# Kernel optimization log

Hardware: AMD Instinct MI355X
Metric: run time of the kernel (lower is better)

## Reference

```python
import jax, jax.numpy as jnp
import numpy as np

D_IN = 1024
D_OUT = 1024

def setup_inputs() -> dict:
    key = jax.random.key(0)
    kx, kq, kk, kv = jax.random.split(key, 4)
    x = jax.random.normal(kx, (4, 4096, D_IN), dtype=jnp.float32)
    s = 1.0 / np.sqrt(D_IN)
    Wq = jax.random.uniform(kq, (D_IN, D_OUT), dtype=jnp.float32, minval=-s, maxval=s)
    Wk = jax.random.uniform(kk, (D_IN, D_OUT), dtype=jnp.float32, minval=-s, maxval=s)
    Wv = jax.random.uniform(kv, (D_IN, D_OUT), dtype=jnp.float32, minval=-s, maxval=s)
    return {"x": x, "Wq": Wq, "Wk": Wk, "Wv": Wv}

def reference(x, Wq, Wk, Wv):
    # x: [B, S, d_in]; single-head causal attention (dropout p=0 => identity)
    B, S, _ = x.shape
    Q = jnp.einsum('bsd,de->bse', x, Wq)
    K = jnp.einsum('bsd,de->bse', x, Wk)
    V = jnp.einsum('bsd,de->bse', x, Wv)
    scale = 1.0 / jnp.sqrt(jnp.asarray(K.shape[-1], dtype=Q.dtype))
    scores = jnp.einsum('bqe,bke->bqk', Q, K) * scale  # [B, S, S]
    causal = jnp.tril(jnp.ones((S, S), dtype=bool))     # mask upper triangle (diag=1)
    scores = jnp.where(causal, scores, -jnp.inf)
    weights = jax.nn.softmax(scores, axis=-1)
    return jnp.einsum('bqk,bke->bqe', weights, V)
```

## Files before the change

### kernel.cpp

```cpp
#include <hip/hip_runtime.h>
#include <hip/hip_bf16.h>
#include <stdint.h>

typedef short short8 __attribute__((ext_vector_type(8)));
typedef short short4v __attribute__((ext_vector_type(4)));
typedef float f32x4 __attribute__((ext_vector_type(4)));

static __device__ __forceinline__ short f2bf(float f) {
  union { float f; uint32_t u; } v; v.f = f;
  uint32_t r = (v.u + 0x7fffu + ((v.u >> 16) & 1u)) >> 16;
  return (short)(uint16_t)r;
}
static __device__ __forceinline__ float bf2f(short h) {
  union { uint32_t u; float f; } v; v.u = ((uint32_t)(uint16_t)h) << 16;
  return v.f;
}

#define MFMA(a, b, c) __builtin_amdgcn_mfma_f32_16x16x32_bf16((a), (b), (c), 0, 0, 0)

static __device__ __forceinline__ void gload16(const short* g, short* l) {
  __builtin_amdgcn_global_load_lds(
      (const __attribute__((address_space(1))) void*)g,
      (__attribute__((address_space(3))) void*)l, 16, 0, 0);
}

static __device__ __forceinline__ void gemm256_ring(
    const short* __restrict__ Ag, int lda,
    const short* __restrict__ Bg, int ldb, int kext,
    short* lds, int t, f32x4 (&acc)[8][4])
{
  const int w = t >> 6, lane = t & 63;
  const int lr = lane & 15, lk = lane >> 4;
  const int wm = w >> 2, wn = w & 3;
  const int nk = kext >> 5;

  const int i0 = t, i1 = 512 + t;
  const int r0 = i0 >> 2, c0 = (i0 & 3) ^ ((r0 >> 1) & 3);
  const int r1 = i1 >> 2, c1 = (i1 & 3) ^ ((r1 >> 1) & 3);
  const short* a0 = Ag + (size_t)r0 * lda + c0 * 8;
  const short* a1 = Ag + (size_t)r1 * lda + c1 * 8;
  const short* b0 = Bg + (size_t)r0 * ldb + c0 * 8;
  const short* b1 = Bg + (size_t)r1 * ldb + c1 * 8;
  const int chq = (lk ^ ((lr >> 1) & 3)) * 8;

#pragma unroll
  for (int p = 0; p < 3; ++p) {
    short* slot = lds + p * 16384;
    gload16(a0 + p * 32, slot + w * 512);
    gload16(a1 + p * 32, slot + 4096 + w * 512);
    gload16(b0 + p * 32, slot + 8192 + w * 512);
    gload16(b1 + p * 32, slot + 12288 + w * 512);
  }
  asm volatile("s_waitcnt vmcnt(8)" ::: "memory");
  __builtin_amdgcn_s_barrier();

  for (int tt = 0; tt < nk; ++tt) {
    short* slot  = lds + (tt & 3) * 16384;
    short* nslot = lds + ((tt + 3) & 3) * 16384;
    const int kk = (tt + 3) << 5;
    const bool st = (tt + 3) < nk;
    short8 bfr[4];

    short8 af[4];
#pragma unroll
    for (int mt = 0; mt < 4; ++mt) {
      int rl = wm * 128 + mt * 16 + lr;
      af[mt] = *(const short8*)&slot[rl * 32 + chq];
    }
#pragma unroll
    for (int nt = 0; nt < 4; ++nt) {
      int rl = wn * 64 + nt * 16 + lr;
      bfr[nt] = *(const short8*)&slot[8192 + rl * 32 + chq];
    }
    if (st) {
      gload16(a0 + kk, nslot + w * 512);
      gload16(a1 + kk, nslot + 4096 + w * 512);
    }
    __builtin_amdgcn_s_barrier();
    asm volatile("s_waitcnt lgkmcnt(0)" ::: "memory");
    __builtin_amdgcn_sched_barrier(0);
    __builtin_amdgcn_s_setprio(1);
#pragma unroll
    for (int mt = 0; mt < 4; ++mt)
#pragma unroll
      for (int nt = 0; nt < 4; ++nt)
        acc[mt][nt] = MFMA(af[mt], bfr[nt], acc[mt][nt]);
    __builtin_amdgcn_s_setprio(0);
    __builtin_amdgcn_s_barrier();

#pragma unroll
    for (int mt = 0; mt < 4; ++mt) {
      int rl = wm * 128 + (4 + mt) * 16 + lr;
      af[mt] = *(const short8*)&slot[rl * 32 + chq];
    }
    if (st) {
      gload16(b0 + kk, nslot + 8192 + w * 512);
      gload16(b1 + kk, nslot + 12288 + w * 512);
    }
    __builtin_amdgcn_s_barrier();
    asm volatile("s_waitcnt lgkmcnt(0)" ::: "memory");
    __builtin_amdgcn_sched_barrier(0);
    __builtin_amdgcn_s_setprio(1);
#pragma unroll
    for (int mt = 0; mt < 4; ++mt)
#pragma unroll
      for (int nt = 0; nt < 4; ++nt)
        acc[4 + mt][nt] = MFMA(af[mt], bfr[nt], acc[4 + mt][nt]);
    __builtin_amdgcn_s_setprio(0);
    const int rem = nk - 1 - tt;
    if (rem >= 3)      { asm volatile("s_waitcnt vmcnt(8)" ::: "memory"); }
    else if (rem == 2) { asm volatile("s_waitcnt vmcnt(4)" ::: "memory"); }
    else if (rem == 1) { asm volatile("s_waitcnt vmcnt(0)" ::: "memory"); }
    __builtin_amdgcn_s_barrier();
  }
}

static __device__ __forceinline__ void gemm_tile128(
    const short* __restrict__ Ag, int lda,
    const short* __restrict__ Bg, int ldb, int kext,
    short* Alds, short* Blds, int w, int lane, f32x4 (&acc)[4][4])
{
  const int wr = (w >> 1) * 64, wc = (w & 1) * 64;
  const int lr = lane & 15, lk = lane >> 4;

  const int c0 = w * 128 + lane;
  const int c1 = c0 + 64;
  const int r0 = c0 >> 2, cg0 = (c0 & 3) ^ ((r0 >> 1) & 3);
  const int r1 = c1 >> 2, cg1 = (c1 & 3) ^ ((r1 >> 1) & 3);
  const short* a0 = Ag + (size_t)r0 * lda + cg0 * 8;
  const short* a1 = Ag + (size_t)r1 * lda + cg1 * 8;
  const short* b0 = Bg + (size_t)r0 * ldb + cg0 * 8;
  const short* b1 = Bg + (size_t)r1 * ldb + cg1 * 8;
  short* la0 = Alds + w * 1024;
  short* la1 = la0 + 512;
  short* lb0 = Blds + w * 1024;
  short* lb1 = lb0 + 512;

  int ra[4], rb[4];
#pragma unroll
  for (int mt = 0; mt < 4; ++mt) {
    int rl = wr + mt * 16 + lr;
    ra[mt] = rl * 32 + (lk ^ ((rl >> 1) & 3)) * 8;
  }
#pragma unroll
  for (int nt = 0; nt < 4; ++nt) {
    int rl = wc + nt * 16 + lr;
    rb[nt] = rl * 32 + (lk ^ ((rl >> 1) & 3)) * 8;
  }

  for (int kk = 0; kk < kext; kk += 32) {
    if (kk) __syncthreads();
    gload16(a0 + kk, la0);
    gload16(a1 + kk, la1);
    gload16(b0 + kk, lb0);
    gload16(b1 + kk, lb1);
    __syncthreads();
    short8 af[4], bfr[4];
#pragma unroll
    for (int mt = 0; mt < 4; ++mt) af[mt] = *(const short8*)&Alds[ra[mt]];
#pragma unroll
    for (int nt = 0; nt < 4; ++nt) bfr[nt] = *(const short8*)&Blds[rb[nt]];
#pragma unroll
    for (int mt = 0; mt < 4; ++mt)
#pragma unroll
      for (int nt = 0; nt < 4; ++nt)
        acc[mt][nt] = MFMA(af[mt], bfr[nt], acc[mt][nt]);
  }
}

__global__ __launch_bounds__(256)
void cvt_x(const float* __restrict__ x, short* __restrict__ xb) {
  size_t i = (size_t)blockIdx.x * 256 + threadIdx.x;
  f32x4 a = *(const f32x4*)(x + i * 8);
  f32x4 b = *(const f32x4*)(x + i * 8 + 4);
  short8 h = { f2bf(a.x), f2bf(a.y), f2bf(a.z), f2bf(a.w),
               f2bf(b.x), f2bf(b.y), f2bf(b.z), f2bf(b.w) };
  *(short8*)(xb + i * 8) = h;
}

__global__ __launch_bounds__(256)
void cvt_w(const float* __restrict__ Wq, const float* __restrict__ Wk,
           const float* __restrict__ Wv, short* __restrict__ wt) {
  __shared__ short Tl[128][136];
  const int z = blockIdx.z;
  const float* W = (z == 0) ? Wq : (z == 1) ? Wk : Wv;
  const float scale = (z == 0) ? 0.03125f : 1.0f;
  const int c0 = blockIdx.x * 128, r0 = blockIdx.y * 128;
  const int t = threadIdx.x;
#pragma unroll
  for (int j = 0; j < 16; ++j) {
    int id = j * 256 + t;
    int row = id >> 5, c4 = id & 31;
    f32x4 v = *(const f32x4*)(W + (size_t)(r0 + row) * 1024 + c0 + c4 * 4);
#pragma unroll
    for (int cc = 0; cc < 4; ++cc) Tl[c4 * 4 + cc][row] = f2bf(v[cc] * scale);
  }
  __syncthreads();
  short* dst = wt + (size_t)z * 1048576;
#pragma unroll
  for (int j = 0; j < 8; ++j) {
    int id = j * 256 + t;
    int col = id >> 4, r8 = id & 15;
    *(short8*)(dst + (size_t)(c0 + col) * 1024 + r0 + r8 * 8) =
        *(const short8*)&Tl[col][r8 * 8];
  }
}

__global__ __launch_bounds__(512, 2)
void qkv_gemm(const short* __restrict__ xb, const short* __restrict__ wt,
              short* __restrict__ q, short* __restrict__ k,
              short* __restrict__ vt) {
  extern __shared__ short lds[];
  const int z = blockIdx.z;
  const int n0 = blockIdx.x * 256, m0 = blockIdx.y * 256;
  const int t = threadIdx.x;
  f32x4 acc[8][4] = {};
  gemm256_ring(xb + (size_t)m0 * 1024, 1024,
               wt + (size_t)z * 1048576 + (size_t)n0 * 1024, 1024, 1024,
               lds, t, acc);
  const int w = t >> 6, lane = t & 63;
  const int lr = lane & 15, lk = lane >> 4;
  const int wm = w >> 2, wn = w & 3;
#pragma unroll
  for (int mt = 0; mt < 8; ++mt) {
#pragma unroll
    for (int nt = 0; nt < 4; ++nt) {
      int col = n0 + wn * 64 + nt * 16 + lr;
      int rbase = m0 + wm * 128 + mt * 16 + lk * 4;
      if (z == 2) {
        int bb = rbase >> 12, s = rbase & 4095;
        short4v h = { f2bf(acc[mt][nt][0]), f2bf(acc[mt][nt][1]),
                      f2bf(acc[mt][nt][2]), f2bf(acc[mt][nt][3]) };
        *(short4v*)(vt + ((size_t)bb * 1024 + col) * 4096 + s) = h;
      } else {
        short* dst = (z == 0) ? q : k;
#pragma unroll
        for (int i = 0; i < 4; ++i)
          dst[(size_t)(rbase + i) * 1024 + col] = f2bf(acc[mt][nt][i]);
      }
    }
  }
}

__global__ __launch_bounds__(512, 2)
void s_gemm(const short* __restrict__ q, const short* __restrict__ k,
            short* __restrict__ P, float* __restrict__ lpart) {
  extern __shared__ short lds[];
  const int bid = blockIdx.x;
  const int b = bid & 3, tt = bid >> 2;
  int ti = (int)((sqrtf(8.f * tt + 1.f) - 1.f) * 0.5f);
  while ((ti + 1) * (ti + 2) / 2 <= tt) ++ti;
  while (ti * (ti + 1) / 2 > tt) --ti;
  const int tj = tt - ti * (ti + 1) / 2;
  const int t = threadIdx.x;
  f32x4 acc[8][4] = {};
  gemm256_ring(q + ((size_t)(b * 4096 + ti * 256)) * 1024, 1024,
               k + ((size_t)(b * 4096 + tj * 256)) * 1024, 1024, 1024,
               lds, t, acc);
  const int w = t >> 6, lane = t & 63;
  const int lr = lane & 15, lk = lane >> 4;
  const int wm = w >> 2, wn = w & 3;
  const bool diag = (ti == tj);
#pragma unroll
  for (int mt = 0; mt < 8; ++mt) {
#pragma unroll
    for (int i = 0; i < 4; ++i) {
      const int rl = wm * 128 + mt * 16 + lk * 4 + i;
      size_t prow = ((size_t)(b * 4096 + ti * 256 + rl)) * 4096 + tj * 256;
      float rs = 0.f;
#pragma unroll
      for (int nt = 0; nt < 4; ++nt) {
        const int cl = wn * 64 + nt * 16 + lr;
        float e = (!diag || cl <= rl) ? __expf(acc[mt][nt][i]) : 0.f;
        short pb = f2bf(e);
        P[prow + cl] = pb;
        rs += bf2f(pb);
      }
      rs += __shfl_xor(rs, 1);
      rs += __shfl_xor(rs, 2);
      rs += __shfl_xor(rs, 4);
      rs += __shfl_xor(rs, 8);
      if (lr == 0)
        lpart[((size_t)(tj * 4 + wn)) * 16384 + b * 4096 + ti * 256 + rl] = rs;
    }
  }
}

__global__ __launch_bounds__(256)
void l_reduce(const float* __restrict__ lpart, float* __restrict__ lsum) {
  int idx = blockIdx.x * 256 + threadIdx.x;
  int qq = idx & 4095;
  int ti = qq >> 8;
  float s = 0.f;
  for (int tj = 0; tj <= ti; ++tj) {
#pragma unroll
    for (int e = 0; e < 4; ++e)
      s += lpart[(size_t)(tj * 4 + e) * 16384 + idx];
  }
  lsum[idx] = s;
}

__global__ __launch_bounds__(256)
void pv_gemm(const short* __restrict__ P, const short* __restrict__ vt,
             const float* __restrict__ lsum, float* __restrict__ out) {
  __shared__ short Alds[128 * 32], Blds[128 * 32];
  const int bid = blockIdx.x;
  const int b = bid & 3;
  const int r = bid >> 2;
  const int dt = r & 7;
  const int qt = 31 - (r >> 3);
  const int t = threadIdx.x, w = t >> 6, lane = t & 63;
  f32x4 acc[4][4] = {};
  gemm_tile128(P + ((size_t)(b * 4096 + qt * 128)) * 4096, 4096,
               vt + ((size_t)(b * 1024 + dt * 128)) * 4096, 4096,
               (qt + 1) * 128, Alds, Blds, w, lane, acc);
  const int lr = lane & 15, lk = lane >> 4;
  const int wr = (w >> 1) * 64, wc = (w & 1) * 64;
#pragma unroll
  for (int mt = 0; mt < 4; ++mt) {
#pragma unroll
    for (int i = 0; i < 4; ++i) {
      int rl = wr + mt * 16 + lk * 4 + i;
      int grow = b * 4096 + qt * 128 + rl;
      float inv = 1.0f / lsum[grow];
#pragma unroll
      for (int nt = 0; nt < 4; ++nt) {
        int cl = wc + nt * 16 + lr;
        out[(size_t)grow * 1024 + dt * 128 + cl] = acc[mt][nt][i] * inv;
      }
    }
  }
}

extern "C" void kernel_launch(void* const* d_in, const int* in_sizes, int n_in,
                              void* d_out, int out_size, void* d_ws, size_t ws_size,
                              hipStream_t stream) {
  (void)in_sizes; (void)n_in; (void)out_size; (void)ws_size;
  const float* x  = (const float*)d_in[0];
  const float* Wq = (const float*)d_in[1];
  const float* Wk = (const float*)d_in[2];
  const float* Wv = (const float*)d_in[3];
  float* out = (float*)d_out;

  short* q_ws  = (short*)d_ws;
  short* k_ws  = q_ws + (size_t)16777216;
  short* vt_ws = k_ws + (size_t)16777216;
  short* P     = vt_ws + (size_t)16777216;
  short* xb    = P;
  float* lpart = (float*)(P + (size_t)67108864);
  float* lsum  = lpart + (size_t)64 * 16384;
  short* wt    = (short*)(lsum + 16384);

  const int gemm_lds = 131072;
  hipFuncSetAttribute((const void*)qkv_gemm,
                      hipFuncAttributeMaxDynamicSharedMemorySize, gemm_lds);
  hipFuncSetAttribute((const void*)s_gemm,
                      hipFuncAttributeMaxDynamicSharedMemorySize, gemm_lds);

  cvt_x<<<dim3(8192), 256, 0, stream>>>(x, xb);
  cvt_w<<<dim3(8, 8, 3), 256, 0, stream>>>(Wq, Wk, Wv, wt);
  qkv_gemm<<<dim3(4, 64, 3), 512, gemm_lds, stream>>>(xb, wt, q_ws, k_ws, vt_ws);
  s_gemm<<<dim3(544), 512, gemm_lds, stream>>>(q_ws, k_ws, P, lpart);
  l_reduce<<<dim3(64), 256, 0, stream>>>(lpart, lsum);
  pv_gemm<<<dim3(1024), 256, 0, stream>>>(P, vt_ws, lsum, out);
}
```

Before: 353.4 us.

## Replace 4-slot K=32 ring with double-buffered K=64 tiles and 4-phase schedule

The shared 256x256 GEMM core drops its 4-deep ring of K=32 slices for two LDS buffers of K=64 slices, using a wider 8-chunk XOR swizzle. Each K step is split into four MFMA phases, and the global-to-LDS loads for the next tile are interleaved across those phases. This halves the number of outer iterations and spreads loads more evenly to cut barrier and wait overhead. The cost is a prefetch depth of only one tile instead of three, so global latency is less hidden, and the fixed vmcnt counts must match the load order exactly.

```diff
diff --git a/kernel.cpp b/kernel.cpp
--- a/kernel.cpp
+++ b/kernel.cpp
@@ -24,7 +24,7 @@
       (__attribute__((address_space(3))) void*)l, 16, 0, 0);
 }
 
-static __device__ __forceinline__ void gemm256_ring(
+static __device__ __forceinline__ void gemm256_m201(
     const short* __restrict__ Ag, int lda,
     const short* __restrict__ Bg, int ldb, int kext,
     short* lds, int t, f32x4 (&acc)[8][4])
@@ -32,50 +32,47 @@
   const int w = t >> 6, lane = t & 63;
   const int lr = lane & 15, lk = lane >> 4;
   const int wm = w >> 2, wn = w & 3;
-  const int nk = kext >> 5;
-
-  const int i0 = t, i1 = 512 + t;
-  const int r0 = i0 >> 2, c0 = (i0 & 3) ^ ((r0 >> 1) & 3);
-  const int r1 = i1 >> 2, c1 = (i1 & 3) ^ ((r1 >> 1) & 3);
-  const short* a0 = Ag + (size_t)r0 * lda + c0 * 8;
-  const short* a1 = Ag + (size_t)r1 * lda + c1 * 8;
-  const short* b0 = Bg + (size_t)r0 * ldb + c0 * 8;
-  const short* b1 = Bg + (size_t)r1 * ldb + c1 * 8;
-  const int chq = (lk ^ ((lr >> 1) & 3)) * 8;
-
-#pragma unroll
-  for (int p = 0; p < 3; ++p) {
-    short* slot = lds + p * 16384;
-    gload16(a0 + p * 32, slot + w * 512);
-    gload16(a1 + p * 32, slot + 4096 + w * 512);
-    gload16(b0 + p * 32, slot + 8192 + w * 512);
-    gload16(b1 + p * 32, slot + 12288 + w * 512);
-  }
-  asm volatile("s_waitcnt vmcnt(8)" ::: "memory");
+  const int nk = kext >> 6;
+
+  short* const Ab0 = lds;
+  short* const Ab1 = lds + 16384;
+  short* const Bb0 = lds + 32768;
+  short* const Bb1 = lds + 49152;
+
+  const int qr = t >> 3;
+  const int qc = (t & 7) ^ (qr & 7);
+  const short* Asrc = Ag + (size_t)qr * lda + qc * 8;
+  const short* Bsrc = Bg + (size_t)qr * ldb + qc * 8;
+
+#define STAGE_A(tile, q) gload16(Asrc + (size_t)(q) * 64 * lda + (tile) * 64, \
+    (((tile) & 1) ? Ab1 : Ab0) + (q) * 4096 + w * 512)
+#define STAGE_B(tile, q) gload16(Bsrc + (size_t)(q) * 64 * ldb + (tile) * 64, \
+    (((tile) & 1) ? Bb1 : Bb0) + (q) * 4096 + w * 512)
+
+  const int chq0 = ((lk) ^ (lr & 7)) * 8;
+  const int chq1 = ((4 + lk) ^ (lr & 7)) * 8;
+  const int arow0 = (wm * 128 + lr) * 64;
+  const int brow0 = (wn * 64 + lr) * 64;
+
+  STAGE_B(0, 0); STAGE_B(0, 2); STAGE_B(0, 1); STAGE_B(0, 3);
+  STAGE_A(0, 0); STAGE_A(0, 2); STAGE_A(0, 1); STAGE_A(0, 3);
+  asm volatile("s_waitcnt vmcnt(2)" ::: "memory");
   __builtin_amdgcn_s_barrier();
 
   for (int tt = 0; tt < nk; ++tt) {
-    short* slot  = lds + (tt & 3) * 16384;
-    short* nslot = lds + ((tt + 3) & 3) * 16384;
-    const int kk = (tt + 3) << 5;
-    const bool st = (tt + 3) < nk;
-    short8 bfr[4];
-
-    short8 af[4];
-#pragma unroll
-    for (int mt = 0; mt < 4; ++mt) {
-      int rl = wm * 128 + mt * 16 + lr;
-      af[mt] = *(const short8*)&slot[rl * 32 + chq];
-    }
-#pragma unroll
-    for (int nt = 0; nt < 4; ++nt) {
-      int rl = wn * 64 + nt * 16 + lr;
-      bfr[nt] = *(const short8*)&slot[8192 + rl * 32 + chq];
-    }
-    if (st) {
-      gload16(a0 + kk, nslot + w * 512);
-      gload16(a1 + kk, nslot + 4096 + w * 512);
-    }
+    const short* Ac = (tt & 1) ? Ab1 : Ab0;
+    const short* Bc = (tt & 1) ? Bb1 : Bb0;
+    const int nx = tt + 1;
+    const bool st = nx < nk;
+    short8 b0[4], b1[4], af[4];
+
+#pragma unroll
+    for (int mt = 0; mt < 4; ++mt)
+      af[mt] = *(const short8*)&Ac[arow0 + mt * 1024 + chq0];
+#pragma unroll
+    for (int nt = 0; nt < 4; ++nt)
+      b0[nt] = *(const short8*)&Bc[brow0 + nt * 1024 + chq0];
+    if (st) { STAGE_B(nx, 0); STAGE_B(nx, 2); }
     __builtin_amdgcn_s_barrier();
     asm volatile("s_waitcnt lgkmcnt(0)" ::: "memory");
     __builtin_amdgcn_sched_barrier(0);
@@ -84,19 +81,17 @@
     for (int mt = 0; mt < 4; ++mt)
 #pragma unroll
       for (int nt = 0; nt < 4; ++nt)
-        acc[mt][nt] = MFMA(af[mt], bfr[nt], acc[mt][nt]);
+        acc[mt][nt] = MFMA(af[mt], b0[nt], acc[mt][nt]);
     __builtin_amdgcn_s_setprio(0);
     __builtin_amdgcn_s_barrier();
 
 #pragma unroll
-    for (int mt = 0; mt < 4; ++mt) {
-      int rl = wm * 128 + (4 + mt) * 16 + lr;
-      af[mt] = *(const short8*)&slot[rl * 32 + chq];
-    }
-    if (st) {
-      gload16(b0 + kk, nslot + 8192 + w * 512);
-      gload16(b1 + kk, nslot + 12288 + w * 512);
-    }
+    for (int mt = 0; mt < 4; ++mt)
+      af[mt] = *(const short8*)&Ac[arow0 + mt * 1024 + chq1];
+#pragma unroll
+    for (int nt = 0; nt < 4; ++nt)
+      b1[nt] = *(const short8*)&Bc[brow0 + nt * 1024 + chq1];
+    if (st) { STAGE_B(nx, 1); STAGE_B(nx, 3); }
     __builtin_amdgcn_s_barrier();
     asm volatile("s_waitcnt lgkmcnt(0)" ::: "memory");
     __builtin_amdgcn_sched_barrier(0);
@@ -105,14 +100,48 @@
     for (int mt = 0; mt < 4; ++mt)
 #pragma unroll
       for (int nt = 0; nt < 4; ++nt)
-        acc[4 + mt][nt] = MFMA(af[mt], bfr[nt], acc[4 + mt][nt]);
+        acc[mt][nt] = MFMA(af[mt], b1[nt], acc[mt][nt]);
     __builtin_amdgcn_s_setprio(0);
-    const int rem = nk - 1 - tt;
-    if (rem >= 3)      { asm volatile("s_waitcnt vmcnt(8)" ::: "memory"); }
-    else if (rem == 2) { asm volatile("s_waitcnt vmcnt(4)" ::: "memory"); }
-    else if (rem == 1) { asm volatile("s_waitcnt vmcnt(0)" ::: "memory"); }
-    __builtin_amdgcn_s_barrier();
-  }
+    if (st) { asm volatile("s_waitcnt vmcnt(4)" ::: "memory"); }
+    else    { asm volatile("s_waitcnt vmcnt(0)" ::: "memory"); }
+    __builtin_amdgcn_s_barrier();
+
+#pragma unroll
+    for (int mt = 0; mt < 4; ++mt)
+      af[mt] = *(const short8*)&Ac[arow0 + 4096 + mt * 1024 + chq0];
+    if (st) { STAGE_A(nx, 0); STAGE_A(nx, 2); }
+    __builtin_amdgcn_s_barrier();
+    asm volatile("s_waitcnt lgkmcnt(0)" ::: "memory");
+    __builtin_amdgcn_sched_barrier(0);
+    __builtin_amdgcn_s_setprio(1);
+#pragma unroll
+    for (int mt = 0; mt < 4; ++mt)
+#pragma unroll
+      for (int nt = 0; nt < 4; ++nt)
+        acc[4 + mt][nt] = MFMA(af[mt], b0[nt], acc[4 + mt][nt]);
+    __builtin_amdgcn_s_setprio(0);
+    __builtin_amdgcn_s_barrier();
+
+#pragma unroll
+    for (int mt = 0; mt < 4; ++mt)
+      af[mt] = *(const short8*)&Ac[arow0 + 4096 + mt * 1024 + chq1];
+    if (st) { STAGE_A(nx, 1); STAGE_A(nx, 3); }
+    __builtin_amdgcn_s_barrier();
+    asm volatile("s_waitcnt lgkmcnt(0)" ::: "memory");
+    __builtin_amdgcn_sched_barrier(0);
+    __builtin_amdgcn_s_setprio(1);
+#pragma unroll
+    for (int mt = 0; mt < 4; ++mt)
+#pragma unroll
+      for (int nt = 0; nt < 4; ++nt)
+        acc[4 + mt][nt] = MFMA(af[mt], b1[nt], acc[4 + mt][nt]);
+    __builtin_amdgcn_s_setprio(0);
+    if (st) { asm volatile("s_waitcnt vmcnt(2)" ::: "memory"); }
+    else    { asm volatile("s_waitcnt vmcnt(0)" ::: "memory"); }
+    __builtin_amdgcn_s_barrier();
+  }
+#undef STAGE_A
+#undef STAGE_B
 }
 
 static __device__ __forceinline__ void gemm_tile128(
@@ -215,7 +244,7 @@
   const int n0 = blockIdx.x * 256, m0 = blockIdx.y * 256;
   const int t = threadIdx.x;
   f32x4 acc[8][4] = {};
-  gemm256_ring(xb + (size_t)m0 * 1024, 1024,
+  gemm256_m201(xb + (size_t)m0 * 1024, 1024,
                wt + (size_t)z * 1048576 + (size_t)n0 * 1024, 1024, 1024,
                lds, t, acc);
   const int w = t >> 6, lane = t & 63;
@@ -254,7 +283,7 @@
   const int tj = tt - ti * (ti + 1) / 2;
   const int t = threadIdx.x;
   f32x4 acc[8][4] = {};
-  gemm256_ring(q + ((size_t)(b * 4096 + ti * 256)) * 1024, 1024,
+  gemm256_m201(q + ((size_t)(b * 4096 + ti * 256)) * 1024, 1024,
                k + ((size_t)(b * 4096 + tj * 256)) * 1024, 1024, 1024,
                lds, t, acc);
   const int w = t >> 6, lane = t & 63;
```

Measured after the change: 339.3 us (median of 2 runs). 1.04x faster.
